# Kernel tuning notes

Hardware: AMD Instinct MI355X
Metric: run time of the kernel (lower is better)

## Reference

```python
import jax, jax.numpy as jnp
from jax import lax
import numpy as np

# DP hyperparameters (from module __init__ defaults)
INS_DEL = 10.0
GAMMA = 1.0
FIRST_CHAR_COST = 10.0


def setup_inputs() -> dict:
    key = jax.random.key(0)
    k1, k2, k3 = jax.random.split(key, 3)
    B, T, M, V = 8192, 16, 16, 256
    tail_logits = jax.random.normal(k1, (B, T, V), dtype=jnp.float32)
    target_idx = jax.random.randint(k2, (B, M), 0, V, dtype=jnp.int32)
    c = jax.random.uniform(k3, (V, V), dtype=jnp.float32)
    # phonetic distance matrix: symmetric, zero diagonal (dist(a,a)=0)
    phon_cost = 0.5 * (c + c.T) * (1.0 - jnp.eye(V, dtype=jnp.float32))
    return {"tail_logits": tail_logits, "target_idx": target_idx, "phon_cost": phon_cost}


def _softmin3(a, b, c, gamma):
    # softmin(a,b,c) = -gamma * log(exp(-a/g)+exp(-b/g)+exp(-c/g))
    x = jnp.stack([a, b, c], axis=0)
    return -gamma * jax.nn.logsumexp(-x / gamma, axis=0)


def _rhyme_dp_loss(tail_logits, target_idx, phon_cost):
    # tail_logits: [B,T,V], target_idx: [B,M] int, phon_cost: [V,V]
    B, T, V = tail_logits.shape
    M = target_idx.shape[1]
    p = jax.nn.softmax(tail_logits, axis=-1)                      # [B,T,V]
    C_cols = phon_cost[:, target_idx]                             # [V,B,M]
    sub = jnp.einsum('btv,vbm->btm', p, C_cols)                   # expected sub cost [B,T,M]

    dt = sub.dtype
    row0 = jnp.broadcast_to(INS_DEL * jnp.arange(M + 1, dtype=dt), (B, M + 1))  # dp[0,:]
    left0s = INS_DEL * jnp.arange(1, T + 1, dtype=dt)             # dp[i,0], i=1..T

    def row_step(prev_row, xs):
        # prev_row: dp[i-1, :] -> [B, M+1]
        sub_i, left0 = xs                                         # sub_i: [B,M]
        init = jnp.full((B,), left0, dtype=dt)                    # dp[i,0]
        cells = (jnp.swapaxes(prev_row[:, 1:], 0, 1),             # up   dp[i-1,j]   [M,B]
                 jnp.swapaxes(prev_row[:, :-1], 0, 1),            # diag dp[i-1,j-1] [M,B]
                 jnp.swapaxes(sub_i, 0, 1))                       # sub[i-1,j-1]     [M,B]

        def cell(left, c):
            up, diag, s = c
            v = _softmin3(up + INS_DEL, left + INS_DEL, diag + s, GAMMA)
            return v, v

        _, vals = lax.scan(cell, init, cells)                     # vals: [M,B]
        row = jnp.concatenate([init[:, None], jnp.swapaxes(vals, 0, 1)], axis=1)
        return row, None

    final_row, _ = lax.scan(row_step, row0, (jnp.swapaxes(sub, 0, 1), left0s))
    dp_TM = final_row[:, -1]                                      # dp[T,M] per pair, [B]

    first_match_prob = jnp.take_along_axis(p[:, 0, :], target_idx[:, :1], axis=1)[:, 0]
    return dp_TM + FIRST_CHAR_COST * (1.0 - first_match_prob)     # [B]


def reference(tail_logits, target_idx, phon_cost):
    return _rhyme_dp_loss(tail_logits, target_idx, phon_cost)
```

## Files before the change

### kernel.cpp

```cpp
#include <hip/hip_runtime.h>

typedef __attribute__((ext_vector_type(8))) short short8;
typedef __attribute__((ext_vector_type(4))) float f32x4;

__device__ __forceinline__ unsigned pk_bf16(float lo, float hi) {
    const unsigned ul = __float_as_uint(lo) + 0x8000u;
    const unsigned uh = __float_as_uint(hi) + 0x8000u;
    return __builtin_amdgcn_perm(uh, ul, 0x07060302u);
}

#define SR 68

__global__ __launch_bounds__(256) void rhyme_kernel(
    const float* __restrict__ logits,
    const int*   __restrict__ tidx,
    const float* __restrict__ phon,
    float*       __restrict__ out,
    int B)
{
    __shared__ __align__(16) unsigned A_l[4][16 * SR];
    __shared__ __align__(16) unsigned B_l[4][16 * SR];
    __shared__ float sub_lds[4][16][17];
    __shared__ float p0e[4];
    __shared__ float p0s[4];

    const int lane = threadIdx.x & 63;
    const int wv   = threadIdx.x >> 6;
    int b = blockIdx.x * 4 + wv;
    if (b >= B) b = B - 1;

    const int t = lane & 15;
    const int q = lane >> 4;

    const int idxn = tidx[b * 16 + t];
    const int idx0 = __shfl(idxn, 0);
    const int h0 = idx0 >> 7;
    const int l0 = (idx0 >> 1) & 63;
    const int e0odd = idx0 & 1;

    unsigned* Aw = &A_l[wv][0];
    unsigned* Bw = &B_l[wv][0];

    union { short8 s; unsigned u[4]; } ones;
    ones.u[0] = ones.u[1] = ones.u[2] = ones.u[3] = 0x3F803F80u;

    f32x4 acc  = {0.f, 0.f, 0.f, 0.f};
    f32x4 accz = {0.f, 0.f, 0.f, 0.f};

    const float* lbase = logits + (size_t)b * 4096;

    for (int h = 0; h < 2; ++h) {
        #pragma unroll
        for (int r = 0; r < 16; ++r) {
            const int row = __shfl(idxn, r);
            const float2 v = *(const float2*)(phon + row * 256 + h * 128 + lane * 2);
            Bw[r * SR + lane] = pk_bf16(v.x, v.y);
        }
        #pragma unroll
        for (int k = 0; k < 16; ++k) {
            const float2 v = *(const float2*)(lbase + k * 256 + h * 128 + lane * 2);
            const float ea = __expf(v.x);
            const float eb = __expf(v.y);
            if (k == 0 && h == h0 && lane == l0)
                p0e[wv] = e0odd ? eb : ea;
            Aw[k * SR + lane] = pk_bf16(ea, eb);
        }
        __asm__ volatile("s_waitcnt lgkmcnt(0)" ::: "memory");

        #pragma unroll
        for (int c = 0; c < 4; ++c) {
            const short8 af = *(const short8*)(Aw + t * SR + c * 16 + q * 4);
            const short8 bf = *(const short8*)(Bw + t * SR + c * 16 + q * 4);
            acc  = __builtin_amdgcn_mfma_f32_16x16x32_bf16(af, bf,     acc,  0, 0, 0);
            accz = __builtin_amdgcn_mfma_f32_16x16x32_bf16(af, ones.s, accz, 0, 0, 0);
        }
        __asm__ volatile("s_waitcnt lgkmcnt(0)" ::: "memory");
    }

    #pragma unroll
    for (int r = 0; r < 4; ++r)
        sub_lds[wv][q * 4 + r][t] = acc[r] / accz[r];

    if (lane == 0)
        p0s[wv] = p0e[wv] / accz[0];

    __syncthreads();
    if (wv != 0) return;

    const int g  = lane >> 4;
    const int tl = lane & 15;
    const int j  = tl + 1;
    float P1 = 0.f, P2 = 0.f;
    #pragma unroll
    for (int d = 2; d <= 32; ++d) {
        const float lnv = __shfl_up(P1, 1);
        const float dgv = __shfl_up(P2, 1);
        const int i = d - j;
        const float up   = (i == 1) ? 10.0f * (float)j : P1;
        const float left = (j == 1) ? 10.0f * (float)i : lnv;
        const float diag = (i == 1) ? 10.0f * (float)(j - 1)
                         : ((j == 1) ? 10.0f * (float)(i - 1) : dgv);
        int row = i - 1; row = row < 0 ? 0 : (row > 15 ? 15 : row);
        const float sv = sub_lds[g][row][tl];
        const float a  = up   + 10.0f;
        const float bc = left + 10.0f;
        const float cc = diag + sv;
        const float mn = fminf(a, fminf(bc, cc));
        const float sm = __expf(mn - a) + __expf(mn - bc) + __expf(mn - cc);
        const float val = mn - __logf(sm);
        const bool act = (i >= 1) && (i <= 16);
        P2 = act ? P1 : P2;
        P1 = act ? val : P1;
    }

    const int gb = blockIdx.x * 4 + g;
    if (tl == 15 && gb < B) {
        out[gb] = P1 + 10.0f * (1.0f - p0s[g]);
    }
}

extern "C" void kernel_launch(void* const* d_in, const int* in_sizes, int n_in,
                              void* d_out, int out_size, void* d_ws, size_t ws_size,
                              hipStream_t stream) {
    const float* logits = (const float*)d_in[0];
    const int*   tidx   = (const int*)d_in[1];
    const float* phon   = (const float*)d_in[2];
    float* out = (float*)d_out;

    const int B = in_sizes[0] / (16 * 256);
    const int blocks = (B + 3) / 4;
    hipLaunchKernelGGL(rhyme_kernel, dim3(blocks), dim3(256), 0, stream,
                       logits, tidx, phon, out, B);
}
```

Measured before the change: 195.5 us.

## Load MFMA operands directly from global memory, dropping LDS staging

Each lane now loads its MFMA A and B fragments straight from global memory as float4 pairs, converting to bf16 in registers. This removes the LDS staging buffers, their waitcnt barriers and the per-row shuffles. The K dimension is permuted consistently for both operands, which is valid because the dot product is order independent. The first-character probability is recomputed with one extra global load. Per-lane loads now stride across rows, which coalesces less well but needs far less LDS.

```diff
diff --git a/kernel.cpp b/kernel.cpp
--- a/kernel.cpp
+++ b/kernel.cpp
@@ -9,8 +9,6 @@
     return __builtin_amdgcn_perm(uh, ul, 0x07060302u);
 }
 
-#define SR 68
-
 __global__ __launch_bounds__(256) void rhyme_kernel(
     const float* __restrict__ logits,
     const int*   __restrict__ tidx,
@@ -18,10 +16,7 @@
     float*       __restrict__ out,
     int B)
 {
-    __shared__ __align__(16) unsigned A_l[4][16 * SR];
-    __shared__ __align__(16) unsigned B_l[4][16 * SR];
     __shared__ float sub_lds[4][16][17];
-    __shared__ float p0e[4];
     __shared__ float p0s[4];
 
     const int lane = threadIdx.x & 63;
@@ -32,14 +27,11 @@
     const int t = lane & 15;
     const int q = lane >> 4;
 
-    const int idxn = tidx[b * 16 + t];
-    const int idx0 = __shfl(idxn, 0);
-    const int h0 = idx0 >> 7;
-    const int l0 = (idx0 >> 1) & 63;
-    const int e0odd = idx0 & 1;
+    const int idxt = tidx[b * 16 + t];
+    const int idx0 = __shfl(idxt, 0);
 
-    unsigned* Aw = &A_l[wv][0];
-    unsigned* Bw = &B_l[wv][0];
+    const float* ap = logits + (size_t)b * 4096 + t * 256 + q * 8;
+    const float* bp = phon + (size_t)idxt * 256 + q * 8;
 
     union { short8 s; unsigned u[4]; } ones;
     ones.u[0] = ones.u[1] = ones.u[2] = ones.u[3] = 0x3F803F80u;
@@ -47,42 +39,35 @@
     f32x4 acc  = {0.f, 0.f, 0.f, 0.f};
     f32x4 accz = {0.f, 0.f, 0.f, 0.f};
 
-    const float* lbase = logits + (size_t)b * 4096;
+    #pragma unroll
+    for (int c = 0; c < 8; ++c) {
+        const float4 a0 = *(const float4*)(ap + c * 32);
+        const float4 a1 = *(const float4*)(ap + c * 32 + 4);
+        const float4 b0 = *(const float4*)(bp + c * 32);
+        const float4 b1 = *(const float4*)(bp + c * 32 + 4);
 
-    for (int h = 0; h < 2; ++h) {
-        #pragma unroll
-        for (int r = 0; r < 16; ++r) {
-            const int row = __shfl(idxn, r);
-            const float2 v = *(const float2*)(phon + row * 256 + h * 128 + lane * 2);
-            Bw[r * SR + lane] = pk_bf16(v.x, v.y);
-        }
-        #pragma unroll
-        for (int k = 0; k < 16; ++k) {
-            const float2 v = *(const float2*)(lbase + k * 256 + h * 128 + lane * 2);
-            const float ea = __expf(v.x);
-            const float eb = __expf(v.y);
-            if (k == 0 && h == h0 && lane == l0)
-                p0e[wv] = e0odd ? eb : ea;
-            Aw[k * SR + lane] = pk_bf16(ea, eb);
-        }
-        __asm__ volatile("s_waitcnt lgkmcnt(0)" ::: "memory");
+        union { short8 s; unsigned u[4]; } af, bf;
+        af.u[0] = pk_bf16(__expf(a0.x), __expf(a0.y));
+        af.u[1] = pk_bf16(__expf(a0.z), __expf(a0.w));
+        af.u[2] = pk_bf16(__expf(a1.x), __expf(a1.y));
+        af.u[3] = pk_bf16(__expf(a1.z), __expf(a1.w));
+        bf.u[0] = pk_bf16(b0.x, b0.y);
+        bf.u[1] = pk_bf16(b0.z, b0.w);
+        bf.u[2] = pk_bf16(b1.x, b1.y);
+        bf.u[3] = pk_bf16(b1.z, b1.w);
 
-        #pragma unroll
-        for (int c = 0; c < 4; ++c) {
-            const short8 af = *(const short8*)(Aw + t * SR + c * 16 + q * 4);
-            const short8 bf = *(const short8*)(Bw + t * SR + c * 16 + q * 4);
-            acc  = __builtin_amdgcn_mfma_f32_16x16x32_bf16(af, bf,     acc,  0, 0, 0);
-            accz = __builtin_amdgcn_mfma_f32_16x16x32_bf16(af, ones.s, accz, 0, 0, 0);
-        }
-        __asm__ volatile("s_waitcnt lgkmcnt(0)" ::: "memory");
+        acc  = __builtin_amdgcn_mfma_f32_16x16x32_bf16(af.s, bf.s,   acc,  0, 0, 0);
+        accz = __builtin_amdgcn_mfma_f32_16x16x32_bf16(af.s, ones.s, accz, 0, 0, 0);
     }
 
     #pragma unroll
     for (int r = 0; r < 4; ++r)
         sub_lds[wv][q * 4 + r][t] = acc[r] / accz[r];
 
-    if (lane == 0)
-        p0s[wv] = p0e[wv] / accz[0];
+    if (lane == 0) {
+        const float p0e = __expf(logits[(size_t)b * 4096 + idx0]);
+        p0s[wv] = p0e / accz[0];
+    }
 
     __syncthreads();
     if (wv != 0) return;
```

After: 198.1 us. No clear change (+1.3%).
